# Optimization experiments

Measured on AMD Instinct MI355X. Metric: run time of the kernel, lower is better.

Reference implementation:

```python
import jax, jax.numpy as jnp
import numpy as np

N_QUERIES = 2000
N_DOCS = 128
FEATURE_DIM = 220
HIDDEN = 768
N_IDS = 65536


def setup_inputs() -> dict:
    key = jax.random.key(0)
    k1, k2, k3, k4, k5 = jax.random.split(key, 5)
    qid = jax.random.randint(k1, (N_IDS,), 0, N_QUERIES)
    did = jax.random.randint(k2, (N_IDS,), 0, N_DOCS)
    input_feature_id = jnp.stack([qid, did], axis=1).astype(jnp.int64)
    feature_table = jax.random.normal(k3, (N_QUERIES, N_DOCS, FEATURE_DIM), dtype=jnp.float32) * 10.0
    W = jax.random.normal(k4, (HIDDEN, FEATURE_DIM), dtype=jnp.float32) * (1.0 / np.sqrt(FEATURE_DIM))
    b = jax.random.normal(k5, (HIDDEN,), dtype=jnp.float32) * 0.01
    return {"input_feature_id": input_feature_id, "feature_table": feature_table, "W": W, "b": b}


def reference(input_feature_id, feature_table, W, b):
    # fused gather over (query, doc) ids: [N, FEATURE_DIM]
    feat = feature_table[input_feature_id[:, 0], input_feature_id[:, 1]]
    # log-sign transform: log(|x| + 1) * sign(x)
    feature_batch = jnp.log(jnp.abs(feat) + 1.0) * jnp.sign(feat)
    # Linear + ReLU (torch Linear: x @ W^T + b)
    output_embeds = jax.nn.relu(feature_batch @ W.T + b)
    return (output_embeds, feature_batch)
```

## Files before the change

### kernel.cpp

```cpp
#include <hip/hip_runtime.h>
#include <hip/hip_bf16.h>

#define M_TOTAL 65536
#define ND      128
#define FDIM    220
#define KPAD    224
#define HID     768
#define CHUNKS  56
#define BSTRIDE 232

using bf16_t = __hip_bfloat16;
using bf16x8 = __attribute__((ext_vector_type(8))) short;
using f32x4  = __attribute__((ext_vector_type(4))) float;

struct __align__(8)  bf4    { bf16_t a, b, c, d; };
struct __align__(16) bf16v8 { bf16_t v[8]; };

__device__ __forceinline__ float slog(float x) {
  return copysignf(log1pf(fabsf(x)), x);
}

__global__ __launch_bounds__(256) void gather_transform_kernel(
    const int* __restrict__ ids, const float* __restrict__ table,
    float* __restrict__ fb_f32, bf16_t* __restrict__ fbB)
{
  int i   = blockIdx.x * 256 + threadIdx.x;
  int row = i / CHUNKS;
  int c4  = i % CHUNKS;
  if (row >= M_TOTAL) return;

  if (c4 == 55) {
    bf4 z; z.a = __float2bfloat16(0.f); z.b = z.a; z.c = z.a; z.d = z.a;
    *(bf4*)(fbB + (size_t)row * KPAD + FDIM) = z;
    return;
  }

  int qid = ids[2 * row];
  int did = ids[2 * row + 1];
  const float4 x =
      *(const float4*)(table + ((size_t)qid * ND + did) * FDIM + c4 * 4);
  float4 y;
  y.x = slog(x.x); y.y = slog(x.y); y.z = slog(x.z); y.w = slog(x.w);
  *(float4*)(fb_f32 + (size_t)row * FDIM + c4 * 4) = y;

  bf4 h;
  h.a = __float2bfloat16(y.x); h.b = __float2bfloat16(y.y);
  h.c = __float2bfloat16(y.z); h.d = __float2bfloat16(y.w);
  *(bf4*)(fbB + (size_t)row * KPAD + c4 * 4) = h;
}

__global__ __launch_bounds__(256, 2) void gemm_bias_relu_kernel(
    const bf16_t* __restrict__ A, const float* __restrict__ W,
    const float* __restrict__ bias, float* __restrict__ out)
{
  __shared__ bf16_t Bs[128 * BSTRIDE];

  const int tid = threadIdx.x;
  const int bn  = blockIdx.x;
  const int bm  = blockIdx.y;

#pragma unroll
  for (int it = 0; it < 14; ++it) {
    const int j   = it * 256 + tid;
    const int row = j / 28;
    const int g   = j % 28;
    const float* src = W + (size_t)(bn * 128 + row) * FDIM + g * 8;
    const float4 f0 = *(const float4*)src;
    float4 f1;
    if (g < 27) {
      f1 = *(const float4*)(src + 4);
    } else {
      f1.x = 0.f; f1.y = 0.f; f1.z = 0.f; f1.w = 0.f;
    }
    bf16v8 h;
    h.v[0] = __float2bfloat16(f0.x); h.v[1] = __float2bfloat16(f0.y);
    h.v[2] = __float2bfloat16(f0.z); h.v[3] = __float2bfloat16(f0.w);
    h.v[4] = __float2bfloat16(f1.x); h.v[5] = __float2bfloat16(f1.y);
    h.v[6] = __float2bfloat16(f1.z); h.v[7] = __float2bfloat16(f1.w);
    *(bf16v8*)(Bs + row * BSTRIDE + g * 8) = h;
  }
  __syncthreads();

  const int wave = tid >> 6;
  const int lane = tid & 63;
  const int wm   = wave & 1;
  const int wn   = wave >> 1;
  const int l15  = lane & 15;
  const int q    = lane >> 4;

  f32x4 acc[4][4];
#pragma unroll
  for (int i = 0; i < 4; ++i)
#pragma unroll
    for (int j = 0; j < 4; ++j) acc[i][j] = (f32x4){0.f, 0.f, 0.f, 0.f};

  const bf16_t* Abase  = A + (size_t)(bm * 128 + wm * 64 + l15) * KPAD + q * 8;
  const bf16_t* BsBase = Bs + (wn * 64 + l15) * BSTRIDE + q * 8;

#pragma unroll
  for (int kb = 0; kb < 7; ++kb) {
    bf16x8 af[4], bg[4];
#pragma unroll
    for (int mi = 0; mi < 4; ++mi)
      af[mi] = *(const bf16x8*)(Abase + (size_t)mi * 16 * KPAD + kb * 32);
#pragma unroll
    for (int ni = 0; ni < 4; ++ni)
      bg[ni] = *(const bf16x8*)(BsBase + ni * 16 * BSTRIDE + kb * 32);
#pragma unroll
    for (int mi = 0; mi < 4; ++mi)
#pragma unroll
      for (int ni = 0; ni < 4; ++ni)
        acc[mi][ni] = __builtin_amdgcn_mfma_f32_16x16x32_bf16(
            af[mi], bg[ni], acc[mi][ni], 0, 0, 0);
  }

  const int col0 = bn * 128 + wn * 64 + l15;
  const int row0 = bm * 128 + wm * 64 + q * 4;
#pragma unroll
  for (int ni = 0; ni < 4; ++ni) {
    const int n    = col0 + ni * 16;
    const float bv = bias[n];
#pragma unroll
    for (int mi = 0; mi < 4; ++mi) {
#pragma unroll
      for (int r = 0; r < 4; ++r) {
        float v = acc[mi][ni][r] + bv;
        out[(size_t)(row0 + mi * 16 + r) * HID + n] = v > 0.f ? v : 0.f;
      }
    }
  }
}

extern "C" void kernel_launch(void* const* d_in, const int* in_sizes, int n_in,
                              void* d_out, int out_size, void* d_ws, size_t ws_size,
                              hipStream_t stream) {
  (void)in_sizes; (void)n_in; (void)out_size; (void)ws_size;

  const int*   ids   = (const int*)d_in[0];
  const float* table = (const float*)d_in[1];
  const float* W     = (const float*)d_in[2];
  const float* bias  = (const float*)d_in[3];

  float* out_embeds = (float*)d_out;
  float* fb_f32     = (float*)d_out + (size_t)M_TOTAL * HID;

  bf16_t* fbB = (bf16_t*)d_ws;

  gather_transform_kernel<<<(M_TOTAL * CHUNKS) / 256, 256, 0, stream>>>(
      ids, table, fb_f32, fbB);

  dim3 grid(HID / 128, M_TOTAL / 128);
  gemm_bias_relu_kernel<<<grid, 256, 0, stream>>>(fbB, W, bias, out_embeds);
}
```

Measured before the change: 438.0 us.

## Drop bf16 workspace copy; convert fp32 features to bf16 inside GEMM

The gather kernel now writes only the fp32 log-sign features, with each thread handling 8 floats, and no longer writes a padded bf16 copy to workspace. The GEMM reads the fp32 features directly and converts them to bf16 in registers, zeroing the K padding. This removes one global write pass and one kernel-side buffer. The cost is that the GEMM's A-operand reads become twice as large and less aligned, and they repeat across the 6 column blocks.

```diff
diff --git a/kernel.cpp b/kernel.cpp
--- a/kernel.cpp
+++ b/kernel.cpp
@@ -4,16 +4,14 @@
 #define M_TOTAL 65536
 #define ND      128
 #define FDIM    220
-#define KPAD    224
 #define HID     768
-#define CHUNKS  56
+#define G8      28
 #define BSTRIDE 232
 
 using bf16_t = __hip_bfloat16;
 using bf16x8 = __attribute__((ext_vector_type(8))) short;
 using f32x4  = __attribute__((ext_vector_type(4))) float;
 
-struct __align__(8)  bf4    { bf16_t a, b, c, d; };
 struct __align__(16) bf16v8 { bf16_t v[8]; };
 
 __device__ __forceinline__ float slog(float x) {
@@ -21,36 +19,32 @@
 }
 
 __global__ __launch_bounds__(256) void gather_transform_kernel(
-    const int* __restrict__ ids, const float* __restrict__ table,
-    float* __restrict__ fb_f32, bf16_t* __restrict__ fbB)
+    const int2* __restrict__ ids, const float* __restrict__ table,
+    float* __restrict__ fb)
 {
-  int i   = blockIdx.x * 256 + threadIdx.x;
-  int row = i / CHUNKS;
-  int c4  = i % CHUNKS;
-  if (row >= M_TOTAL) return;
+  const int j   = blockIdx.x * 256 + threadIdx.x;
+  const int row = j / G8;
+  const int g   = j % G8;
 
-  if (c4 == 55) {
-    bf4 z; z.a = __float2bfloat16(0.f); z.b = z.a; z.c = z.a; z.d = z.a;
-    *(bf4*)(fbB + (size_t)row * KPAD + FDIM) = z;
-    return;
+  const int2 p = ids[row];
+  const float* src = table + ((size_t)p.x * ND + p.y) * FDIM + g * 8;
+  float*       dst = fb + (size_t)row * FDIM + g * 8;
+
+  const float4 f0 = *(const float4*)src;
+  float4 y0;
+  y0.x = slog(f0.x); y0.y = slog(f0.y); y0.z = slog(f0.z); y0.w = slog(f0.w);
+  *(float4*)dst = y0;
+
+  if (g < 27) {
+    const float4 f1 = *(const float4*)(src + 4);
+    float4 y1;
+    y1.x = slog(f1.x); y1.y = slog(f1.y); y1.z = slog(f1.z); y1.w = slog(f1.w);
+    *(float4*)(dst + 4) = y1;
   }
-
-  int qid = ids[2 * row];
-  int did = ids[2 * row + 1];
-  const float4 x =
-      *(const float4*)(table + ((size_t)qid * ND + did) * FDIM + c4 * 4);
-  float4 y;
-  y.x = slog(x.x); y.y = slog(x.y); y.z = slog(x.z); y.w = slog(x.w);
-  *(float4*)(fb_f32 + (size_t)row * FDIM + c4 * 4) = y;
-
-  bf4 h;
-  h.a = __float2bfloat16(y.x); h.b = __float2bfloat16(y.y);
-  h.c = __float2bfloat16(y.z); h.d = __float2bfloat16(y.w);
-  *(bf4*)(fbB + (size_t)row * KPAD + c4 * 4) = h;
 }
 
 __global__ __launch_bounds__(256, 2) void gemm_bias_relu_kernel(
-    const bf16_t* __restrict__ A, const float* __restrict__ W,
+    const float* __restrict__ A, const float* __restrict__ W,
     const float* __restrict__ bias, float* __restrict__ out)
 {
   __shared__ bf16_t Bs[128 * BSTRIDE];
@@ -61,9 +55,9 @@
 
 #pragma unroll
   for (int it = 0; it < 14; ++it) {
-    const int j   = it * 256 + tid;
-    const int row = j / 28;
-    const int g   = j % 28;
+    const int jj  = it * 256 + tid;
+    const int row = jj / 28;
+    const int g   = jj % 28;
     const float* src = W + (size_t)(bn * 128 + row) * FDIM + g * 8;
     const float4 f0 = *(const float4*)src;
     float4 f1;
@@ -94,15 +88,29 @@
 #pragma unroll
     for (int j = 0; j < 4; ++j) acc[i][j] = (f32x4){0.f, 0.f, 0.f, 0.f};
 
-  const bf16_t* Abase  = A + (size_t)(bm * 128 + wm * 64 + l15) * KPAD + q * 8;
+  const float*  Abase  = A + (size_t)(bm * 128 + wm * 64 + l15) * FDIM + q * 8;
   const bf16_t* BsBase = Bs + (wn * 64 + l15) * BSTRIDE + q * 8;
 
 #pragma unroll
   for (int kb = 0; kb < 7; ++kb) {
     bf16x8 af[4], bg[4];
 #pragma unroll
-    for (int mi = 0; mi < 4; ++mi)
-      af[mi] = *(const bf16x8*)(Abase + (size_t)mi * 16 * KPAD + kb * 32);
+    for (int mi = 0; mi < 4; ++mi) {
+      const float* ap = Abase + (size_t)mi * 16 * FDIM + kb * 32;
+      const float4 f0 = *(const float4*)ap;
+      float4 f1;
+      if (kb == 6 && q == 3) {
+        f1.x = 0.f; f1.y = 0.f; f1.z = 0.f; f1.w = 0.f;
+      } else {
+        f1 = *(const float4*)(ap + 4);
+      }
+      bf16v8 h;
+      h.v[0] = __float2bfloat16(f0.x); h.v[1] = __float2bfloat16(f0.y);
+      h.v[2] = __float2bfloat16(f0.z); h.v[3] = __float2bfloat16(f0.w);
+      h.v[4] = __float2bfloat16(f1.x); h.v[5] = __float2bfloat16(f1.y);
+      h.v[6] = __float2bfloat16(f1.z); h.v[7] = __float2bfloat16(f1.w);
+      af[mi] = *(const bf16x8*)&h;
+    }
 #pragma unroll
     for (int ni = 0; ni < 4; ++ni)
       bg[ni] = *(const bf16x8*)(BsBase + ni * 16 * BSTRIDE + kb * 32);
@@ -134,9 +142,9 @@
 extern "C" void kernel_launch(void* const* d_in, const int* in_sizes, int n_in,
                               void* d_out, int out_size, void* d_ws, size_t ws_size,
                               hipStream_t stream) {
-  (void)in_sizes; (void)n_in; (void)out_size; (void)ws_size;
+  (void)in_sizes; (void)n_in; (void)out_size; (void)d_ws; (void)ws_size;
 
-  const int*   ids   = (const int*)d_in[0];
+  const int2*  ids   = (const int2*)d_in[0];
   const float* table = (const float*)d_in[1];
   const float* W     = (const float*)d_in[2];
   const float* bias  = (const float*)d_in[3];
@@ -144,11 +152,9 @@
   float* out_embeds = (float*)d_out;
   float* fb_f32     = (float*)d_out + (size_t)M_TOTAL * HID;
 
-  bf16_t* fbB = (bf16_t*)d_ws;
-
-  gather_transform_kernel<<<(M_TOTAL * CHUNKS) / 256, 256, 0, stream>>>(
-      ids, table, fb_f32, fbB);
+  gather_transform_kernel<<<(M_TOTAL * G8) / 256, 256, 0, stream>>>(
+      ids, table, fb_f32);
 
   dim3 grid(HID / 128, M_TOTAL / 128);
-  gemm_bias_relu_kernel<<<grid, 256, 0, stream>>>(fbB, W, bias, out_embeds);
+  gemm_bias_relu_kernel<<<grid, 256, 0, stream>>>(fb_f32, W, bias, out_embeds);
 }
```

After: 473.1 us. 1.08x slower.
